# Kernel optimization log

Hardware: AMD Instinct MI355X
Metric: run time of the kernel (lower is better)

Reference implementation:

```python
import jax, jax.numpy as jnp
import numpy as np

B, S, D = 2, 2048, 1024
H = 16
HD = D // H  # 64

def setup_inputs() -> dict:
    key = jax.random.key(0)
    ks = jax.random.split(key, 6)
    s = 1.0 / np.sqrt(D)
    return {
        "x": jax.random.normal(ks[0], (B, S, D), dtype=jnp.float32),
        "Wq": jax.random.normal(ks[1], (D, D), dtype=jnp.float32) * s,
        "Wk": jax.random.normal(ks[2], (D, D), dtype=jnp.float32) * s,
        "Wv": jax.random.normal(ks[3], (D, D), dtype=jnp.float32) * s,
        "Wo": jax.random.normal(ks[4], (D, D), dtype=jnp.float32) * s,
        "bo": jax.random.normal(ks[5], (D,), dtype=jnp.float32) * 0.01,
    }

def reference(x, Wq, Wk, Wv, Wo, bo):
    b, n, _ = x.shape
    # qkv projections (nn.Linear: x @ W^T, no bias for qkv)
    q = (x @ Wq.T).reshape(b, n, H, HD).transpose(0, 2, 1, 3)  # [B,H,S,hd]
    k = (x @ Wk.T).reshape(b, n, H, HD).transpose(0, 2, 1, 3)
    v = (x @ Wv.T).reshape(b, n, H, HD).transpose(0, 2, 1, 3)
    scores = jnp.einsum('bhqd,bhkd->bhqk', q, k)  # [B,H,S,S]
    causal = jnp.triu(jnp.ones((n, n), dtype=bool), k=1)
    scores = jnp.where(causal, -jnp.inf, scores)
    attn = jax.nn.softmax(scores / np.sqrt(HD), axis=-1)
    ctx = jnp.einsum('bhqk,bhkd->bhqd', attn, v)  # [B,H,S,hd]
    ctx = ctx.transpose(0, 2, 1, 3).reshape(b, n, D)
    return ctx @ Wo.T + bo
```

## Files before the change

kernel.cpp:

```cpp
#include <hip/hip_runtime.h>
#include <hip/hip_bf16.h>

typedef __hip_bfloat16 bf16;
typedef short v8s __attribute__((ext_vector_type(8)));
typedef float v4f __attribute__((ext_vector_type(4)));
typedef float v16f __attribute__((ext_vector_type(16)));

#define S_ 2048
#define D_ 1024
#define H_ 16
#define HD_ 64

#define EXP2F(x) __builtin_amdgcn_exp2f(x)
#define NEG_BIG (-1.0e30f)
#define C2 0.1803368801111244f

#define GLDS16(g, l) __builtin_amdgcn_global_load_lds(                        \
    (const __attribute__((address_space(1))) unsigned int*)(g),               \
    (__attribute__((address_space(3))) unsigned int*)(l), 16, 0, 0)

#define CVT_PK(d, lo, hi) \
    asm("v_cvt_pk_bf16_f32 %0, %1, %2" : "=v"(d) : "v"(lo), "v"(hi))

#define SWAPHALF(a, b) \
    asm("v_permlane32_swap_b32 %0, %1" : "+v"(a), "+v"(b))

#define MFMA32(a, b, c) __builtin_amdgcn_mfma_f32_32x32x16_bf16(a, b, c, 0, 0, 0)

static __device__ __forceinline__ unsigned short bf16_bits(bf16 h) {
    union { bf16 h; unsigned short u; } c; c.h = h; return c.u;
}

static __device__ __forceinline__ v8s pack_bf16x8(const float4 a, const float4 b) {
    union { v8s v; unsigned short u[8]; } r;
    r.u[0] = bf16_bits(__float2bfloat16(a.x));
    r.u[1] = bf16_bits(__float2bfloat16(a.y));
    r.u[2] = bf16_bits(__float2bfloat16(a.z));
    r.u[3] = bf16_bits(__float2bfloat16(a.w));
    r.u[4] = bf16_bits(__float2bfloat16(b.x));
    r.u[5] = bf16_bits(__float2bfloat16(b.y));
    r.u[6] = bf16_bits(__float2bfloat16(b.z));
    r.u[7] = bf16_bits(__float2bfloat16(b.w));
    return r.v;
}

__global__ __launch_bounds__(256)
void cvt_bf16(const float* __restrict__ x,  const float* __restrict__ wq,
              const float* __restrict__ wk, const float* __restrict__ wv,
              const float* __restrict__ wo,
              bf16* __restrict__ xb,  bf16* __restrict__ wqb,
              bf16* __restrict__ wkb, bf16* __restrict__ wvb,
              bf16* __restrict__ wob)
{
    const int seg = blockIdx.y;
    const float* src; bf16* dst; int n;
    switch (seg) {
        case 0: src = x;  dst = xb;  n = 4096 * 1024; break;
        case 1: src = wq; dst = wqb; n = 1024 * 1024; break;
        case 2: src = wk; dst = wkb; n = 1024 * 1024; break;
        case 3: src = wv; dst = wvb; n = 1024 * 1024; break;
        default:src = wo; dst = wob; n = 1024 * 1024; break;
    }
    const int idx = (blockIdx.x * 256 + threadIdx.x) * 8;
    if (idx >= n) return;
    *(v8s*)&dst[idx] = pack_bf16x8(*(const float4*)&src[idx],
                                   *(const float4*)&src[idx + 4]);
}

static __device__ __forceinline__ void stage_half(bf16* ldsbase, const bf16* gbase,
                                                  int w, int l) {
    const int r = l >> 3, c = ((l & 7) ^ r) * 8;
    GLDS16(gbase + (size_t)((2 * w + 0) * 8 + r) * 1024 + c, ldsbase + (2 * w + 0) * 512);
    GLDS16(gbase + (size_t)((2 * w + 1) * 8 + r) * 1024 + c, ldsbase + (2 * w + 1) * 512);
}

#define MF16(a, b, c) __builtin_amdgcn_mfma_f32_16x16x32_bf16(a, b, c, 0, 0, 0)

#define LDA(buf, mf0) { _Pragma("unroll") for (int m_ = 0; m_ < 4; ++m_) {          \
    af[m_][0] = *(const v8s*)&AsS[(buf)*16384 + abase + ((mf0) + m_)*1024 + sw0];   \
    af[m_][1] = *(const v8s*)&AsS[(buf)*16384 + abase + ((mf0) + m_)*1024 + sw1]; } }
#define LDB0(buf) { _Pragma("unroll") for (int n_ = 0; n_ < 2; ++n_) {              \
    b0f[n_][0] = *(const v8s*)&BsS[(buf)*16384 + bbase + n_*1024 + sw0];            \
    b0f[n_][1] = *(const v8s*)&BsS[(buf)*16384 + bbase + n_*1024 + sw1]; } }
#define LDB1(buf) { _Pragma("unroll") for (int n_ = 0; n_ < 2; ++n_) {              \
    b1f[n_][0] = *(const v8s*)&BsS[(buf)*16384 + bbase + (2 + n_)*1024 + sw0];      \
    b1f[n_][1] = *(const v8s*)&BsS[(buf)*16384 + bbase + (2 + n_)*1024 + sw1]; } }
#define MMQ(MH, NH, AF, BF) { _Pragma("unroll") for (int m_ = 0; m_ < 4; ++m_)      \
    _Pragma("unroll") for (int n_ = 0; n_ < 2; ++n_) {                              \
      acc[(MH)*4 + m_][(NH)*2 + n_] =                                               \
        MF16(AF[m_][0], BF[n_][0], acc[(MH)*4 + m_][(NH)*2 + n_]);                  \
      acc[(MH)*4 + m_][(NH)*2 + n_] =                                               \
        MF16(AF[m_][1], BF[n_][1], acc[(MH)*4 + m_][(NH)*2 + n_]); } }
#define BAR() __builtin_amdgcn_s_barrier()
#define VMC2() asm volatile("s_waitcnt vmcnt(2)" ::: "memory")
#define PRIO1() __builtin_amdgcn_s_setprio(1)
#define PRIO0() __builtin_amdgcn_s_setprio(0)

__global__ __launch_bounds__(512, 2)
void gemm_qkv_8p(const bf16* __restrict__ xb, const bf16* __restrict__ wqb,
                 const bf16* __restrict__ wkb, const bf16* __restrict__ wvb,
                 bf16* __restrict__ qd, bf16* __restrict__ kd, bf16* __restrict__ vtd)
{
    __shared__ bf16 AsS[2 * 16384];
    __shared__ bf16 BsS[2 * 16384];
    const int mode = blockIdx.z;
    const bf16* __restrict__ W = (mode == 0) ? wqb : (mode == 1) ? wkb : wvb;
    const int m0 = blockIdx.x * 256;
    const int n0 = blockIdx.y * 256;
    const int t = threadIdx.x;
    const int lane = t & 63, w = t >> 6;
    const int wr = w >> 2, wc = w & 3;
    const int l15 = lane & 15, quad = lane >> 4;
    const int sw0 = (quad ^ (l15 & 7)) * 8;
    const int sw1 = ((quad + 4) ^ (l15 & 7)) * 8;
    const int abase = wr * 8192 + l15 * 64;
    const int bbase = (wc >> 1) * 8192 + (wc & 1) * 4096 + l15 * 64;
    const bf16* Aap = xb + (size_t)m0 * 1024;
    const bf16* Bbp = W + (size_t)n0 * 1024;

    v4f acc[8][4] = {};
    v8s af[4][2], b0f[2][2], b1f[2][2];

    stage_half(AsS,          Aap,          w, lane);
    stage_half(AsS + 8192,   Aap + 131072, w, lane);
    stage_half(BsS,          Bbp,          w, lane);
    stage_half(BsS + 8192,   Bbp + 131072, w, lane);
    stage_half(AsS + 16384,  Aap + 64,     w, lane);
    VMC2();
    BAR();

    for (int i = 0; i < 8; ++i) {
        const int kc = i * 128;
        LDA(0, 0); LDB0(0);
        stage_half(AsS + 16384 + 8192, Aap + 131072 + kc + 64, w, lane);
        BAR(); PRIO1(); MMQ(0, 0, af, b0f); PRIO0(); BAR();
        LDB1(0);
        stage_half(BsS + 16384, Bbp + kc + 64, w, lane);
        BAR(); PRIO1(); MMQ(0, 1, af, b1f); PRIO0(); BAR();
        LDA(0, 4);
        stage_half(BsS + 16384 + 8192, Bbp + 131072 + kc + 64, w, lane);
        BAR(); PRIO1(); MMQ(1, 1, af, b1f); PRIO0(); BAR();
        stage_half(AsS, Aap + kc + 128, w, lane);
        VMC2();
        BAR(); PRIO1(); MMQ(1, 0, af, b0f); PRIO0(); BAR();
        LDA(1, 0); LDB0(1);
        stage_half(AsS + 8192, Aap + 131072 + kc + 128, w, lane);
        BAR(); PRIO1(); MMQ(0, 0, af, b0f); PRIO0(); BAR();
        LDB1(1);
        stage_half(BsS, Bbp + kc + 128, w, lane);
        BAR(); PRIO1(); MMQ(0, 1, af, b1f); PRIO0(); BAR();
        LDA(1, 4);
        stage_half(BsS + 8192, Bbp + 131072 + kc + 128, w, lane);
        BAR(); PRIO1(); MMQ(1, 1, af, b1f); PRIO0(); BAR();
        stage_half(AsS + 16384, Aap + kc + 192, w, lane);
        VMC2();
        BAR(); PRIO1(); MMQ(1, 0, af, b0f); PRIO0(); BAR();
    }

    const float qscale = (mode == 0) ? C2 : 1.0f;
#pragma unroll
    for (int mf = 0; mf < 8; ++mf) {
        const int mb = m0 + wr * 128 + mf * 16 + quad * 4;
        const int b_ = mb >> 11, s = mb & 2047;
#pragma unroll
        for (int nf = 0; nf < 4; ++nf) {
            const int n = n0 + wc * 64 + nf * 16 + l15;
            const int h = n >> 6, d = n & 63;
            if (mode == 2) {
                unsigned int lo = (unsigned int)bf16_bits(__float2bfloat16(acc[mf][nf][0]))
                                | ((unsigned int)bf16_bits(__float2bfloat16(acc[mf][nf][1])) << 16);
                unsigned int hi = (unsigned int)bf16_bits(__float2bfloat16(acc[mf][nf][2]))
                                | ((unsigned int)bf16_bits(__float2bfloat16(acc[mf][nf][3])) << 16);
                uint2 pv; pv.x = lo; pv.y = hi;
                *(uint2*)&vtd[((b_ * H_ + h) * HD_ + d) * S_ + s] = pv;
            } else {
                bf16* __restrict__ dst = (mode == 0) ? qd : kd;
#pragma unroll
                for (int r = 0; r < 4; ++r)
                    dst[((b_ * H_ + h) * S_ + (s + r)) * HD_ + d] =
                        __float2bfloat16(acc[mf][nf][r] * qscale);
            }
        }
    }
}

__global__ __launch_bounds__(256)
void gemm_out_f(const bf16* __restrict__ ctx, const bf16* __restrict__ wob,
                const float* __restrict__ bo, float* __restrict__ out)
{
    const int m0 = blockIdx.x * 128;
    const int n0 = blockIdx.y * 128;
    __shared__ bf16 As[128 * 32];
    __shared__ bf16 Bs[128 * 32];
    const int t    = threadIdx.x;
    const int lane = t & 63, w = t >> 6;
    const int wr = w >> 1, wc = w & 1;
    const int l15 = lane & 15, quad = lane >> 4;
    const int r16 = lane >> 2, c8 = (lane & 3) * 8;
    v4f acc[4][4] = {};

    const bf16* ga = &ctx[(m0 + w*16 + r16) * 1024 + c8];
    const bf16* gb = &wob[(n0 + w*16 + r16) * 1024 + c8];
    bf16* la0 = &As[w * 16 * 32];
    bf16* la1 = &As[(64 + w * 16) * 32];
    bf16* lb0 = &Bs[w * 16 * 32];
    bf16* lb1 = &Bs[(64 + w * 16) * 32];

    for (int k0 = 0; k0 < 1024; k0 += 32) {
        __syncthreads();
        GLDS16(ga + k0,             la0);
        GLDS16(ga + k0 + 64 * 1024, la1);
        GLDS16(gb + k0,             lb0);
        GLDS16(gb + k0 + 64 * 1024, lb1);
        __syncthreads();
        v8s a[4], b[4];
#pragma unroll
        for (int mt = 0; mt < 4; mt++) a[mt] = *(const v8s*)&As[(wr*64 + mt*16 + l15)*32 + quad*8];
#pragma unroll
        for (int nt = 0; nt < 4; nt++) b[nt] = *(const v8s*)&Bs[(wc*64 + nt*16 + l15)*32 + quad*8];
#pragma unroll
        for (int mt = 0; mt < 4; mt++)
#pragma unroll
            for (int nt = 0; nt < 4; nt++)
                acc[mt][nt] = __builtin_amdgcn_mfma_f32_16x16x32_bf16(a[mt], b[nt], acc[mt][nt], 0, 0, 0);
    }

#pragma unroll
    for (int mt = 0; mt < 4; mt++) {
        const int mb = m0 + wr*64 + mt*16 + quad*4;
#pragma unroll
        for (int nt = 0; nt < 4; nt++) {
            const int n = n0 + wc*64 + nt*16 + l15;
            const float bias = bo[n];
#pragma unroll
            for (int r = 0; r < 4; r++)
                out[(mb + r)*1024 + n] = acc[mt][nt][r] + bias;
        }
    }
}

__global__ __launch_bounds__(256)
void gemm_qkv(const float* __restrict__ x, const float* __restrict__ Wq,
              const float* __restrict__ Wk, const float* __restrict__ Wv,
              bf16* __restrict__ qd, bf16* __restrict__ kd, bf16* __restrict__ vtd)
{
    const int mode = blockIdx.z;
    const float* __restrict__ W = (mode == 0) ? Wq : (mode == 1) ? Wk : Wv;
    const int m0 = blockIdx.x * 128;
    const int n0 = blockIdx.y * 128;
    __shared__ bf16 As[128 * 40];
    __shared__ bf16 Bs[128 * 40];
    const int t    = threadIdx.x;
    const int lane = t & 63, w = t >> 6;
    const int wr = w >> 1, wc = w & 1;
    const int l15 = lane & 15, quad = lane >> 4;
    const int srow = t >> 2, scol = (t & 3) * 8;
    v4f acc[4][4] = {};

    for (int k0 = 0; k0 < 1024; k0 += 32) {
        __syncthreads();
        {
            const float* pa = &x[(m0 + srow) * 1024 + k0 + scol];
            *(v8s*)&As[srow*40 + scol] = pack_bf16x8(*(const float4*)pa, *(const float4*)(pa + 4));
            const float* pa2 = pa + 64 * 1024;
            *(v8s*)&As[(srow+64)*40 + scol] = pack_bf16x8(*(const float4*)pa2, *(const float4*)(pa2 + 4));
            const float* pb = &W[(n0 + srow) * 1024 + k0 + scol];
            *(v8s*)&Bs[srow*40 + scol] = pack_bf16x8(*(const float4*)pb, *(const float4*)(pb + 4));
            const float* pb2 = pb + 64 * 1024;
            *(v8s*)&Bs[(srow+64)*40 + scol] = pack_bf16x8(*(const float4*)pb2, *(const float4*)(pb2 + 4));
        }
        __syncthreads();
        v8s a[4], b[4];
#pragma unroll
        for (int mt = 0; mt < 4; mt++) a[mt] = *(const v8s*)&As[(wr*64 + mt*16 + l15)*40 + quad*8];
#pragma unroll
        for (int nt = 0; nt < 4; nt++) b[nt] = *(const v8s*)&Bs[(wc*64 + nt*16 + l15)*40 + quad*8];
#pragma unroll
        for (int mt = 0; mt < 4; mt++)
#pragma unroll
            for (int nt = 0; nt < 4; nt++)
                acc[mt][nt] = __builtin_amdgcn_mfma_f32_16x16x32_bf16(a[mt], b[nt], acc[mt][nt], 0, 0, 0);
    }

    const float qscale = (mode == 0) ? C2 : 1.0f;
#pragma unroll
    for (int mt = 0; mt < 4; mt++) {
        const int mb = m0 + wr*64 + mt*16 + quad*4;
        const int b_ = mb >> 11, s = mb & 2047;
#pragma unroll
        for (int nt = 0; nt < 4; nt++) {
            const int n = n0 + wc*64 + nt*16 + l15;
            const int h = n >> 6, d = n & 63;
            if (mode == 2) {
                unsigned int lo = (unsigned int)bf16_bits(__float2bfloat16(acc[mt][nt][0]))
                                | ((unsigned int)bf16_bits(__float2bfloat16(acc[mt][nt][1])) << 16);
                unsigned int hi = (unsigned int)bf16_bits(__float2bfloat16(acc[mt][nt][2]))
                                | ((unsigned int)bf16_bits(__float2bfloat16(acc[mt][nt][3])) << 16);
                uint2 pv; pv.x = lo; pv.y = hi;
                *(uint2*)&vtd[((b_*H_ + h)*HD_ + d)*S_ + s] = pv;
            } else {
                bf16* __restrict__ dst = (mode == 0) ? qd : kd;
#pragma unroll
                for (int r = 0; r < 4; r++)
                    dst[((b_*H_ + h)*S_ + (s + r))*HD_ + d] = __float2bfloat16(acc[mt][nt][r] * qscale);
            }
        }
    }
}

__global__ __launch_bounds__(256)
void gemm_out(const bf16* __restrict__ ctx, const float* __restrict__ Wo,
              const float* __restrict__ bo, float* __restrict__ out)
{
    const int m0 = blockIdx.x * 128;
    const int n0 = blockIdx.y * 128;
    __shared__ bf16 As[128 * 40];
    __shared__ bf16 Bs[128 * 40];
    const int t    = threadIdx.x;
    const int lane = t & 63, w = t >> 6;
    const int wr = w >> 1, wc = w & 1;
    const int l15 = lane & 15, quad = lane >> 4;
    const int srow = t >> 2, scol = (t & 3) * 8;
    v4f acc[4][4] = {};

    for (int k0 = 0; k0 < 1024; k0 += 32) {
        __syncthreads();
        {
            *(v8s*)&As[srow*40 + scol]      = *(const v8s*)&ctx[(m0+srow)*1024 + k0 + scol];
            *(v8s*)&As[(srow+64)*40 + scol] = *(const v8s*)&ctx[(m0+srow+64)*1024 + k0 + scol];
            const float* pb = &Wo[(n0 + srow) * 1024 + k0 + scol];
            *(v8s*)&Bs[srow*40 + scol] = pack_bf16x8(*(const float4*)pb, *(const float4*)(pb + 4));
            const float* pb2 = pb + 64 * 1024;
            *(v8s*)&Bs[(srow+64)*40 + scol] = pack_bf16x8(*(const float4*)pb2, *(const float4*)(pb2 + 4));
        }
        __syncthreads();
        v8s a[4], b[4];
#pragma unroll
        for (int mt = 0; mt < 4; mt++) a[mt] = *(const v8s*)&As[(wr*64 + mt*16 + l15)*40 + quad*8];
#pragma unroll
        for (int nt = 0; nt < 4; nt++) b[nt] = *(const v8s*)&Bs[(wc*64 + nt*16 + l15)*40 + quad*8];
#pragma unroll
        for (int mt = 0; mt < 4; mt++)
#pragma unroll
            for (int nt = 0; nt < 4; nt++)
                acc[mt][nt] = __builtin_amdgcn_mfma_f32_16x16x32_bf16(a[mt], b[nt], acc[mt][nt], 0, 0, 0);
    }

#pragma unroll
    for (int mt = 0; mt < 4; mt++) {
        const int mb = m0 + wr*64 + mt*16 + quad*4;
#pragma unroll
        for (int nt = 0; nt < 4; nt++) {
            const int n = n0 + wc*64 + nt*16 + l15;
            const float bias = bo[n];
#pragma unroll
            for (int r = 0; r < 4; r++)
                out[(mb + r)*1024 + n] = acc[mt][nt][r] + bias;
        }
    }
}

#define SOFTMAX_PV(sa, ks0, vA0, vA1, vB0, vB1)                                \
    {                                                                          \
        const bool full_ = ((ks0) + 31 <= q0w);                                \
        if (full_) {                                                           \
            _Pragma("unroll")                                                  \
            for (int r = 0; r < 16; r++) {                                     \
                const float p = EXP2F(sa[r]); sa[r] = p;                       \
                if (r & 1) ps1 += p; else ps0 += p;                            \
            }                                                                  \
        } else {                                                               \
            const int kb_ = (ks0) + 4 * hi - q0w - l31;                        \
            _Pragma("unroll")                                                  \
            for (int r = 0; r < 16; r++) {                                     \
                const int kl_ = (r & 3) + 8 * (r >> 2);                        \
                const float p = EXP2F((kb_ + kl_ <= 0) ? sa[r] : NEG_BIG);     \
                sa[r] = p;                                                     \
                if (r & 1) ps1 += p; else ps0 += p;                            \
            }                                                                  \
        }                                                                      \
        unsigned u0, u1, u2, u3, u4, u5, u6, u7;                               \
        CVT_PK(u0, sa[0],  sa[1]);  CVT_PK(u1, sa[2],  sa[3]);                 \
        CVT_PK(u2, sa[4],  sa[5]);  CVT_PK(u3, sa[6],  sa[7]);                 \
        CVT_PK(u4, sa[8],  sa[9]);  CVT_PK(u5, sa[10], sa[11]);                \
        CVT_PK(u6, sa[12], sa[13]); CVT_PK(u7, sa[14], sa[15]);                \
        SWAPHALF(u0, u2); SWAPHALF(u1, u3);                                    \
        SWAPHALF(u4, u6); SWAPHALF(u5, u7);                                    \
        union { v8s v; unsigned w[4]; } pa0_, pa1_;                            \
        pa0_.w[0] = u0; pa0_.w[1] = u1; pa0_.w[2] = u2; pa0_.w[3] = u3;        \
        pa1_.w[0] = u4; pa1_.w[1] = u5; pa1_.w[2] = u6; pa1_.w[3] = u7;        \
        o0 = MFMA32(pa0_.v, vA0, o0);                                          \
        o1 = MFMA32(pa0_.v, vB0, o1);                                          \
        o0 = MFMA32(pa1_.v, vA1, o0);                                          \
        o1 = MFMA32(pa1_.v, vB1, o1);                                          \
    }

__global__ __launch_bounds__(512)
void flash_attn(const bf16* __restrict__ qd, const bf16* __restrict__ kd,
                const bf16* __restrict__ vtd, bf16* __restrict__ ctx)
{
    const int bh = blockIdx.x;
    const int p  = blockIdx.y;
    const int t = threadIdx.x;
    const int lane = t & 63, w = t >> 6;
    const int l31 = lane & 31, hi = lane >> 5;
    const int side = w >> 2, wl = w & 3;
    const int q0w = (side ? (15 - p) : p) * 128 + wl * 32;
    const int nT = 16 - p;

    __shared__ bf16 Vs[2][64 * 136];

    const bf16* qp = qd + ((size_t)bh * S_ + q0w + l31) * HD_ + hi * 8;
    const v8s qf0 = *(const v8s*)(qp);
    const v8s qf1 = *(const v8s*)(qp + 16);
    const v8s qf2 = *(const v8s*)(qp + 32);
    const v8s qf3 = *(const v8s*)(qp + 48);

    v16f o0 = {}, o1 = {};
    float ps0 = 0.f, ps1 = 0.f;

    const int vrow = t >> 3, vcol = (t & 7) * 8;
    const bf16* vp = vtd + ((size_t)bh * HD_ + vrow) * S_ + vcol;
    v8s pv0 = *(const v8s*)vp;
    v8s pv1 = *(const v8s*)(vp + 64);

    const bf16* kq = kd + ((size_t)bh * S_ + l31) * HD_ + hi * 8;
    v8s kA0 = *(const v8s*)(kq);
    v8s kA1 = *(const v8s*)(kq + 16);
    v8s kA2 = *(const v8s*)(kq + 32);
    v8s kA3 = *(const v8s*)(kq + 48);
    v8s kB0 = *(const v8s*)(kq + 32 * HD_);
    v8s kB1 = *(const v8s*)(kq + 32 * HD_ + 16);
    v8s kB2 = *(const v8s*)(kq + 32 * HD_ + 32);
    v8s kB3 = *(const v8s*)(kq + 32 * HD_ + 48);

    for (int it = 0; it < nT; ++it) {
        const int c0 = it * 128;
        bf16* Vb = &Vs[it & 1][0];
        *(v8s*)&Vb[vrow*136 + vcol]      = pv0;
        *(v8s*)&Vb[vrow*136 + 64 + vcol] = pv1;
        __syncthreads();
        vp += 128;
        pv0 = *(const v8s*)vp;
        pv1 = *(const v8s*)(vp + 64);

#pragma unroll
        for (int h = 0; h < 2; ++h) {
            const int ch = c0 + h * 64;
            const bool actA = (ch      <= q0w + 31);
            const bool actB = (ch + 32 <= q0w + 31);
            const bool nact = (ch + 64 <= q0w + 31);

            v16f sa0 = {}, sa1 = {};
            if (actA) {
                sa0 = MFMA32(kA0, qf0, sa0);
                sa0 = MFMA32(kA1, qf1, sa0);
                sa0 = MFMA32(kA2, qf2, sa0);
                sa0 = MFMA32(kA3, qf3, sa0);
            }
            if (actB) {
                sa1 = MFMA32(kB0, qf0, sa1);
                sa1 = MFMA32(kB1, qf1, sa1);
                sa1 = MFMA32(kB2, qf2, sa1);
                sa1 = MFMA32(kB3, qf3, sa1);
            }

            if (nact) {
                const bf16* kn = kq + (size_t)(ch + 64) * HD_;
                kA0 = *(const v8s*)(kn);
                kA1 = *(const v8s*)(kn + 16);
                kA2 = *(const v8s*)(kn + 32);
                kA3 = *(const v8s*)(kn + 48);
                kB0 = *(const v8s*)(kn + 32 * HD_);
                kB1 = *(const v8s*)(kn + 32 * HD_ + 16);
                kB2 = *(const v8s*)(kn + 32 * HD_ + 32);
                kB3 = *(const v8s*)(kn + 32 * HD_ + 48);
            }

            if (actA) {
                const int kb = h * 64;
                const v8s vA0 = *(const v8s*)&Vb[ l31      *136 + kb      + hi*8];
                const v8s vA1 = *(const v8s*)&Vb[ l31      *136 + kb + 16 + hi*8];
                const v8s vB0 = *(const v8s*)&Vb[(l31 + 32)*136 + kb      + hi*8];
                const v8s vB1 = *(const v8s*)&Vb[(l31 + 32)*136 + kb + 16 + hi*8];
                SOFTMAX_PV(sa0, ch, vA0, vA1, vB0, vB1);
            }
            if (actB) {
                const int kb = h * 64 + 32;
                const v8s vA2 = *(const v8s*)&Vb[ l31      *136 + kb      + hi*8];
                const v8s vA3 = *(const v8s*)&Vb[ l31      *136 + kb + 16 + hi*8];
                const v8s vB2 = *(const v8s*)&Vb[(l31 + 32)*136 + kb      + hi*8];
                const v8s vB3 = *(const v8s*)&Vb[(l31 + 32)*136 + kb + 16 + hi*8];
                SOFTMAX_PV(sa1, ch + 32, vA2, vA3, vB2, vB3);
            }
        }
    }

    const float ps = ps0 + ps1;
    const float tot = ps + __shfl_xor(ps, 32);
    const int b_ = bh >> 4, hh = bh & 15;
    bf16* cb = ctx + ((size_t)b_ * S_ + q0w) * D_ + hh * HD_ + l31;
#pragma unroll
    for (int r = 0; r < 16; r++) {
        const int qr = (r & 3) + 8 * (r >> 2) + 4 * hi;
        const float linv = 1.0f / __shfl(tot, qr);
        cb[(size_t)qr * D_]      = __float2bfloat16(o0[r] * linv);
        cb[(size_t)qr * D_ + 32] = __float2bfloat16(o1[r] * linv);
    }
}

extern "C" void kernel_launch(void* const* d_in, const int* in_sizes, int n_in,
                              void* d_out, int out_size, void* d_ws, size_t ws_size,
                              hipStream_t stream) {
    const float* x  = (const float*)d_in[0];
    const float* Wq = (const float*)d_in[1];
    const float* Wk = (const float*)d_in[2];
    const float* Wv = (const float*)d_in[3];
    const float* Wo = (const float*)d_in[4];
    const float* bo = (const float*)d_in[5];
    float* out = (float*)d_out;

    const size_t SEG = (size_t)2 * H_ * S_ * HD_;
    bf16* qd  = (bf16*)d_ws;
    bf16* kd  = qd  + SEG;
    bf16* vtd = kd  + SEG;
    bf16* xc  = vtd + SEG;
    bf16* wqb = xc + SEG;
    bf16* wkb = wqb + 1024 * 1024;
    bf16* wvb = wkb + 1024 * 1024;
    bf16* wob = wvb + 1024 * 1024;

    const size_t need_fast = (4 * SEG + 4 * 1024 * 1024) * sizeof(bf16);

    if (ws_size >= need_fast) {
        cvt_bf16<<<dim3(2048, 5), 256, 0, stream>>>(x, Wq, Wk, Wv, Wo,
                                                    xc, wqb, wkb, wvb, wob);
        gemm_qkv_8p<<<dim3(16, 4, 3), 512, 0, stream>>>(xc, wqb, wkb, wvb, qd, kd, vtd);
        flash_attn<<<dim3(32, 8), 512, 0, stream>>>(qd, kd, vtd, xc);
        gemm_out_f<<<dim3(32, 8), 256, 0, stream>>>(xc, wob, bo, out);
    } else {
        gemm_qkv<<<dim3(32, 8, 3), 256, 0, stream>>>(x, Wq, Wk, Wv, qd, kd, vtd);
        flash_attn<<<dim3(32, 8), 512, 0, stream>>>(qd, kd, vtd, xc);
        gemm_out<<<dim3(32, 8), 256, 0, stream>>>(xc, Wo, bo, out);
    }
}
```

Before: 187.8 us.

## Split attention KV range across two wave groups and merge partial outputs

Each block now handles one 128-row query tile instead of pairing tile p with tile 15-p. The two 4-wave halves split the key range, each taking alternating 128-key chunks, and the side-1 partial accumulators and row sums are reduced through shared memory at the end. The grid doubles to 16 tiles per head, heavier tiles are launched first, and launch bounds request 4 waves per SIMD. The aim is more parallelism and better load balance, at the cost of double the V staging in LDS, an extra reduction step and possible register pressure. The merge simply adds the two partial sums, which assumes the softmax uses a fixed (non-running) max.

Result: slower. 306.6 us (+63.3%).

```diff
diff --git a/kernel.cpp b/kernel.cpp
--- a/kernel.cpp
+++ b/kernel.cpp
@@ -395,20 +395,20 @@
         o1 = MFMA32(pa1_.v, vB1, o1);                                          \
     }
 
-__global__ __launch_bounds__(512)
+__global__ __launch_bounds__(512, 4)
 void flash_attn(const bf16* __restrict__ qd, const bf16* __restrict__ kd,
                 const bf16* __restrict__ vtd, bf16* __restrict__ ctx)
 {
     const int bh = blockIdx.x;
-    const int p  = blockIdx.y;
+    const int p  = 15 - (int)blockIdx.y;
     const int t = threadIdx.x;
     const int lane = t & 63, w = t >> 6;
     const int l31 = lane & 31, hi = lane >> 5;
     const int side = w >> 2, wl = w & 3;
-    const int q0w = (side ? (15 - p) : p) * 128 + wl * 32;
-    const int nT = 16 - p;
-
-    __shared__ bf16 Vs[2][64 * 136];
+    const int q0w = p * 128 + wl * 32;
+    const int nIt = (p + 2) >> 1;
+
+    __shared__ bf16 Vs[2][2][64 * 136];
 
     const bf16* qp = qd + ((size_t)bh * S_ + q0w + l31) * HD_ + hi * 8;
     const v8s qf0 = *(const v8s*)(qp);
@@ -423,33 +423,44 @@
     const bf16* vp = vtd + ((size_t)bh * HD_ + vrow) * S_ + vcol;
     v8s pv0 = *(const v8s*)vp;
     v8s pv1 = *(const v8s*)(vp + 64);
+    v8s pv2 = *(const v8s*)(vp + 128);
+    v8s pv3 = *(const v8s*)(vp + 192);
 
     const bf16* kq = kd + ((size_t)bh * S_ + l31) * HD_ + hi * 8;
-    v8s kA0 = *(const v8s*)(kq);
-    v8s kA1 = *(const v8s*)(kq + 16);
-    v8s kA2 = *(const v8s*)(kq + 32);
-    v8s kA3 = *(const v8s*)(kq + 48);
-    v8s kB0 = *(const v8s*)(kq + 32 * HD_);
-    v8s kB1 = *(const v8s*)(kq + 32 * HD_ + 16);
-    v8s kB2 = *(const v8s*)(kq + 32 * HD_ + 32);
-    v8s kB3 = *(const v8s*)(kq + 32 * HD_ + 48);
-
-    for (int it = 0; it < nT; ++it) {
-        const int c0 = it * 128;
-        bf16* Vb = &Vs[it & 1][0];
-        *(v8s*)&Vb[vrow*136 + vcol]      = pv0;
-        *(v8s*)&Vb[vrow*136 + 64 + vcol] = pv1;
-        __syncthreads();
-        vp += 128;
+    const bf16* kq0 = kq + (size_t)(128 * side) * HD_;
+    v8s kA0 = *(const v8s*)(kq0);
+    v8s kA1 = *(const v8s*)(kq0 + 16);
+    v8s kA2 = *(const v8s*)(kq0 + 32);
+    v8s kA3 = *(const v8s*)(kq0 + 48);
+    v8s kB0 = *(const v8s*)(kq0 + 32 * HD_);
+    v8s kB1 = *(const v8s*)(kq0 + 32 * HD_ + 16);
+    v8s kB2 = *(const v8s*)(kq0 + 32 * HD_ + 32);
+    v8s kB3 = *(const v8s*)(kq0 + 32 * HD_ + 48);
+
+    for (int it = 0; it < nIt; ++it) {
+        bf16* Vb0 = &Vs[it & 1][0][0];
+        bf16* Vb1 = &Vs[it & 1][1][0];
+        *(v8s*)&Vb0[vrow*136 + vcol]      = pv0;
+        *(v8s*)&Vb0[vrow*136 + 64 + vcol] = pv1;
+        *(v8s*)&Vb1[vrow*136 + vcol]      = pv2;
+        *(v8s*)&Vb1[vrow*136 + 64 + vcol] = pv3;
+        __syncthreads();
+        vp += 256;
         pv0 = *(const v8s*)vp;
         pv1 = *(const v8s*)(vp + 64);
+        pv2 = *(const v8s*)(vp + 128);
+        pv3 = *(const v8s*)(vp + 192);
+
+        const int c0 = it * 256 + side * 128;
+        bf16* Vb = side ? Vb1 : Vb0;
 
 #pragma unroll
         for (int h = 0; h < 2; ++h) {
             const int ch = c0 + h * 64;
+            const int nko = h ? 192 : 64;
             const bool actA = (ch      <= q0w + 31);
             const bool actB = (ch + 32 <= q0w + 31);
-            const bool nact = (ch + 64 <= q0w + 31);
+            const bool nact = (ch + nko <= q0w + 31);
 
             v16f sa0 = {}, sa1 = {};
             if (actA) {
@@ -466,7 +477,7 @@
             }
 
             if (nact) {
-                const bf16* kn = kq + (size_t)(ch + 64) * HD_;
+                const bf16* kn = kq + (size_t)(ch + nko) * HD_;
                 kA0 = *(const v8s*)(kn);
                 kA1 = *(const v8s*)(kn + 16);
                 kA2 = *(const v8s*)(kn + 32);
@@ -496,16 +507,40 @@
         }
     }
 
-    const float ps = ps0 + ps1;
-    const float tot = ps + __shfl_xor(ps, 32);
-    const int b_ = bh >> 4, hh = bh & 15;
-    bf16* cb = ctx + ((size_t)b_ * S_ + q0w) * D_ + hh * HD_ + l31;
-#pragma unroll
-    for (int r = 0; r < 16; r++) {
-        const int qr = (r & 3) + 8 * (r >> 2) + 4 * hi;
-        const float linv = 1.0f / __shfl(tot, qr);
-        cb[(size_t)qr * D_]      = __float2bfloat16(o0[r] * linv);
-        cb[(size_t)qr * D_ + 32] = __float2bfloat16(o1[r] * linv);
+    __syncthreads();
+    float* sm = (float*)&Vs[0][0][0];
+    const int slot = (wl * 64 + lane) * 36;
+    if (side) {
+#pragma unroll
+        for (int c = 0; c < 4; ++c) {
+            v4f t0, t1;
+#pragma unroll
+            for (int j = 0; j < 4; ++j) { t0[j] = o0[c*4+j]; t1[j] = o1[c*4+j]; }
+            *(v4f*)&sm[slot + c*4]      = t0;
+            *(v4f*)&sm[slot + 16 + c*4] = t1;
+        }
+        sm[slot + 32] = ps0 + ps1;
+    }
+    __syncthreads();
+    if (!side) {
+#pragma unroll
+        for (int c = 0; c < 4; ++c) {
+            const v4f t0 = *(const v4f*)&sm[slot + c*4];
+            const v4f t1 = *(const v4f*)&sm[slot + 16 + c*4];
+#pragma unroll
+            for (int j = 0; j < 4; ++j) { o0[c*4+j] += t0[j]; o1[c*4+j] += t1[j]; }
+        }
+        const float ps = ps0 + ps1 + sm[slot + 32];
+        const float tot = ps + __shfl_xor(ps, 32);
+        const int b_ = bh >> 4, hh = bh & 15;
+        bf16* cb = ctx + ((size_t)b_ * S_ + q0w) * D_ + hh * HD_ + l31;
+#pragma unroll
+        for (int r = 0; r < 16; r++) {
+            const int qr = (r & 3) + 8 * (r >> 2) + 4 * hi;
+            const float linv = 1.0f / __shfl(tot, qr);
+            cb[(size_t)qr * D_]      = __float2bfloat16(o0[r] * linv);
+            cb[(size_t)qr * D_ + 32] = __float2bfloat16(o1[r] * linv);
+        }
     }
 }
 
@@ -536,11 +571,11 @@
         cvt_bf16<<<dim3(2048, 5), 256, 0, stream>>>(x, Wq, Wk, Wv, Wo,
                                                     xc, wqb, wkb, wvb, wob);
         gemm_qkv_8p<<<dim3(16, 4, 3), 512, 0, stream>>>(xc, wqb, wkb, wvb, qd, kd, vtd);
-        flash_attn<<<dim3(32, 8), 512, 0, stream>>>(qd, kd, vtd, xc);
+        flash_attn<<<dim3(32, 16), 512, 0, stream>>>(qd, kd, vtd, xc);
         gemm_out_f<<<dim3(32, 8), 256, 0, stream>>>(xc, wob, bo, out);
     } else {
         gemm_qkv<<<dim3(32, 8, 3), 256, 0, stream>>>(x, Wq, Wk, Wv, qd, kd, vtd);
-        flash_attn<<<dim3(32, 8), 512, 0, stream>>>(qd, kd, vtd, xc);
+        flash_attn<<<dim3(32, 16), 512, 0, stream>>>(qd, kd, vtd, xc);
         gemm_out<<<dim3(32, 8), 256, 0, stream>>>(xc, Wo, bo, out);
     }
 }
```
